# Performance work log

Measured on AMD Instinct MI355X. Metric: run time of the kernel, lower is better.

Reference implementation:

```python
import jax, jax.numpy as jnp
import numpy as np

NEG_SLOPE = 0.2
EPS = 1e-8

def add_self_loops(edge_index, n_nodes):
    loops = jnp.arange(n_nodes, dtype=edge_index.dtype)
    return jnp.concatenate([edge_index, jnp.stack([loops, loops])], axis=1)

def gatv2_layer(x, edge_index, Wl, Wr, att, bias, concat):
    # x: [N, Fin], edge_index: [2, E] (row0=src j, row1=dst i), att: [H, Fout]
    N = x.shape[0]
    H, Fo = att.shape
    ei = add_self_loops(edge_index, N)
    src, dst = ei[0], ei[1]
    xl = (x @ Wl).reshape(N, H, Fo)
    xr = (x @ Wr).reshape(N, H, Fo)
    s = xl[src] + xr[dst]                                   # [E, H, Fo]
    e = jnp.einsum('ehf,hf->eh', jax.nn.leaky_relu(s, NEG_SLOPE), att)  # [E, H]
    # segment softmax over edges sharing the same destination node
    m = jax.ops.segment_max(e, dst, num_segments=N)          # [N, H]
    ex = jnp.exp(e - m[dst])
    den = jax.ops.segment_sum(ex, dst, num_segments=N)
    alpha = ex / (den[dst] + 1e-16)                          # [E, H]
    out = jax.ops.segment_sum(xl[src] * alpha[:, :, None], dst, num_segments=N)  # [N, H, Fo]
    out = out.reshape(N, H * Fo) if concat else out.mean(axis=1)
    return out + bias

def forward_once(x, edge_index, W1l, W1r, att1, b1, W2l, W2r, att2, b2):
    # eval mode: dropouts are identity
    h = jax.nn.elu(gatv2_layer(x, edge_index, W1l, W1r, att1, b1, concat=True))
    return gatv2_layer(h, edge_index, W2l, W2r, att2, b2, concat=False)

def reference(x1, edge_index1, x2, edge_index2, W1l, W1r, att1, b1, W2l, W2r, att2, b2):
    y = forward_once(x1, edge_index1, W1l, W1r, att1, b1, W2l, W2r, att2, b2)
    z = forward_once(x2, edge_index2, W1l, W1r, att1, b1, W2l, W2r, att2, b2)
    logp_y = jax.nn.log_softmax(y, axis=1)
    logp_z = jax.nn.log_softmax(z, axis=1)
    ny = jnp.maximum(jnp.linalg.norm(y, axis=1), EPS)
    nz = jnp.maximum(jnp.linalg.norm(z, axis=1), EPS)
    cos = jnp.sum(y * z, axis=1) / (ny * nz)
    return (logp_y, 1.0 - cos, logp_z, logp_y, logp_y)

def setup_inputs() -> dict:
    key = jax.random.key(0)
    ks = jax.random.split(key, 12)
    N, E, Fin, HID, H, C = 50000, 800000, 256, 32, 8, 16
    g = lambda k, shape, fan: jax.random.normal(k, shape, jnp.float32) * (1.0 / np.sqrt(fan))
    return {
        'x1': jax.random.normal(ks[0], (N, Fin), jnp.float32),
        'edge_index1': jax.random.randint(ks[1], (2, E), 0, N, jnp.int32),
        'x2': jax.random.normal(ks[2], (N, Fin), jnp.float32),
        'edge_index2': jax.random.randint(ks[3], (2, E), 0, N, jnp.int32),
        'W1l': g(ks[4], (Fin, H * HID), Fin),
        'W1r': g(ks[5], (Fin, H * HID), Fin),
        'att1': g(ks[6], (H, HID), HID),
        'b1': jnp.zeros((H * HID,), jnp.float32),
        'W2l': g(ks[7], (H * HID, 1 * C), H * HID),
        'W2r': g(ks[8], (H * HID, 1 * C), H * HID),
        'att2': g(ks[9], (1, C), C),
        'b2': jnp.zeros((C,), jnp.float32),
    }
```

## Files before the change

### kernel.cpp

```cpp
#include <hip/hip_runtime.h>
#include <hip/hip_bf16.h>
#include <math.h>

#define FIN 256
#define C2  16
#define NEG 0.2f
#define LOG2E 1.4426950408889634f

typedef short bf16x8 __attribute__((ext_vector_type(8)));
typedef float f32x4v __attribute__((ext_vector_type(4)));
typedef float f32x2 __attribute__((ext_vector_type(2)));

__device__ __forceinline__ float bf2f(unsigned short u) {
  union { float f; unsigned int i; } c; c.i = ((unsigned int)u) << 16; return c.f;
}
__device__ __forceinline__ unsigned short f2bf(float f) {
  __hip_bfloat16 b = __float2bfloat16(f);
  return *(unsigned short*)&b;
}
__device__ __forceinline__ f32x2 bfpair(unsigned int u) {
  union { float f; unsigned int i; } lo, hi;
  lo.i = u << 16;
  hi.i = u & 0xffff0000u;
  f32x2 r; r.x = lo.f; r.y = hi.f; return r;
}

__global__ __launch_bounds__(256) void deg_kernel(const int* __restrict__ ei1,
    const int* __restrict__ ei2, int* __restrict__ deg, int E, int N) {
  int EQ = (E + 3) >> 2;
  int q = blockIdx.x * 256 + threadIdx.x;
  if (q >= 2 * EQ) return;
  int g = q >= EQ;
  int lq = g ? q - EQ : q;
  const int* dstp = (g ? ei2 : ei1) + E;
  int base = g * N;
  int e0 = lq * 4;
  if (e0 + 3 < E) {
    int4 d4 = *(const int4*)&dstp[e0];
    atomicAdd(&deg[base + d4.x], 1);
    atomicAdd(&deg[base + d4.y], 1);
    atomicAdd(&deg[base + d4.z], 1);
    atomicAdd(&deg[base + d4.w], 1);
  } else {
    for (int k = 0; k < 4 && e0 + k < E; k++)
      atomicAdd(&deg[base + dstp[e0 + k]], 1);
  }
}

__global__ __launch_bounds__(1024) void scan_part_kernel(const int* __restrict__ deg,
    int* __restrict__ offs, int* __restrict__ partials, int n) {
  __shared__ int wsum[16], wpref[16];
  int tid = threadIdx.x, lane = tid & 63, wid = tid >> 6;
  int idx = blockIdx.x * 1024 + tid;
  int v = (idx < n) ? deg[idx] : 0;
  int s = v;
#pragma unroll
  for (int o = 1; o < 64; o <<= 1) {
    int t = __shfl_up(s, o, 64);
    if (lane >= o) s += t;
  }
  if (lane == 63) wsum[wid] = s;
  __syncthreads();
  if (tid < 16) {
    int t = wsum[tid];
    int ss = t;
#pragma unroll
    for (int o = 1; o < 16; o <<= 1) {
      int u = __shfl_up(ss, o, 16);
      if (tid >= o) ss += u;
    }
    wpref[tid] = ss - t;
    if (tid == 15) partials[blockIdx.x] = ss;
  }
  __syncthreads();
  if (idx < n) offs[idx] = wpref[wid] + s - v;
}

__global__ __launch_bounds__(1024) void scan_fix_kernel(int* __restrict__ offs,
    const int* __restrict__ partials, int nb, int n) {
  __shared__ int wsum[16], wpref[16];
  __shared__ int carry_s;
  int tid = threadIdx.x, lane = tid & 63, wid = tid >> 6;
  int v = (tid < nb) ? partials[tid] : 0;
  int s = v;
#pragma unroll
  for (int o = 1; o < 64; o <<= 1) {
    int t = __shfl_up(s, o, 64);
    if (lane >= o) s += t;
  }
  if (lane == 63) wsum[wid] = s;
  __syncthreads();
  if (tid < 16) {
    int t = wsum[tid];
    int ss = t;
#pragma unroll
    for (int o = 1; o < 16; o <<= 1) {
      int u = __shfl_up(ss, o, 16);
      if (tid >= o) ss += u;
    }
    wpref[tid] = ss - t;
  }
  __syncthreads();
  s += wpref[wid];
  int b = blockIdx.x;
  if (b == 0) {
    if (tid == nb - 1) offs[n] = s;
  } else if (tid == b - 1) {
    carry_s = s;
  }
  __syncthreads();
  if (b > 0) {
    int idx = b * 1024 + tid;
    if (idx < n) offs[idx] += carry_s;
  }
}

__global__ __launch_bounds__(256) void fill_kernel(const int* __restrict__ ei1,
    const int* __restrict__ ei2, const int* __restrict__ offs,
    int* __restrict__ cnt, int* __restrict__ csr, int E, int N) {
  int EQ = (E + 3) >> 2;
  int q = blockIdx.x * 256 + threadIdx.x;
  if (q >= 2 * EQ) return;
  int g = q >= EQ;
  int lq = g ? q - EQ : q;
  const int* ei = g ? ei2 : ei1;
  int base = g * N;
  int e0 = lq * 4;
  if (e0 + 3 < E) {
    int4 s4 = *(const int4*)&ei[e0];
    int4 d4 = *(const int4*)&ei[E + e0];
    int n0 = base + d4.x, n1 = base + d4.y, n2 = base + d4.z, n3 = base + d4.w;
    csr[offs[n0] + atomicAdd(&cnt[n0], 1)] = base + s4.x;
    csr[offs[n1] + atomicAdd(&cnt[n1], 1)] = base + s4.y;
    csr[offs[n2] + atomicAdd(&cnt[n2], 1)] = base + s4.z;
    csr[offs[n3] + atomicAdd(&cnt[n3], 1)] = base + s4.w;
  } else {
    for (int k = 0; k < 4 && e0 + k < E; k++) {
      int node = base + ei[E + e0 + k];
      csr[offs[node] + atomicAdd(&cnt[node], 1)] = base + ei[e0 + k];
    }
  }
}

__global__ __launch_bounds__(256) void cvt_w_kernel(const float* __restrict__ W1l,
    const float* __restrict__ W1r, const float* __restrict__ W2l,
    const float* __restrict__ W2r, unsigned short* __restrict__ Wt,
    unsigned short* __restrict__ Wt2) {
  int n = blockIdx.x;
  int k = threadIdx.x;
  if (n < 512) {
    float v = (n < 256) ? W1l[k * 256 + n] : W1r[k * 256 + (n - 256)];
    Wt[n * 256 + k] = f2bf(v);
  } else {
    int c = n - 512;
    float v = (c < 16) ? W2l[k * 16 + c] : W2r[k * 16 + (c - 16)];
    Wt2[c * 256 + k] = f2bf(v);
  }
}

#define LDT 72
__global__ __launch_bounds__(512) void gemm_mfma_kernel(
    const float* __restrict__ X1, const float* __restrict__ X2,
    const unsigned short* __restrict__ Bt,
    unsigned short* __restrict__ xlb, unsigned short* __restrict__ xrb,
    int M, int NN) {
  __shared__ __align__(16) unsigned short As[128 * LDT];
  __shared__ __align__(16) unsigned short Bs[128 * LDT];
  int tid = threadIdx.x;
  int G = gridDim.x;
  int q = G >> 3, r = G & 7;
  int b = blockIdx.x;
  int xcd = b & 7, pos = b >> 3;
  int swz = (xcd < r) ? xcd * (q + 1) + pos : r * (q + 1) + (xcd - r) * q + pos;
  int row0 = (swz >> 2) * 128;
  int col0 = (swz & 3) * 128;
  int wid = tid >> 6, lane = tid & 63;
  int wr = wid >> 2, wc = wid & 3;
  int r16 = lane & 15, kb = (lane >> 4) * 8;

  f32x4v acc[4][2];
#pragma unroll
  for (int m = 0; m < 4; m++)
#pragma unroll
    for (int n = 0; n < 2; n++)
#pragma unroll
      for (int qq = 0; qq < 4; qq++) acc[m][n][qq] = 0.f;

  for (int k0 = 0; k0 < 256; k0 += 64) {
#pragma unroll
    for (int it = 0; it < 2; it++) {
      int g = tid + it * 512;
      int rr = g >> 3;
      int ko = (g & 7) * 8;
      int gr = row0 + rr;
      float4 a0 = make_float4(0.f, 0.f, 0.f, 0.f);
      float4 a1 = make_float4(0.f, 0.f, 0.f, 0.f);
      if (gr < M) {
        const float* src = (gr < NN) ? &X1[(size_t)gr * 256]
                                     : &X2[(size_t)(gr - NN) * 256];
        a0 = *(const float4*)&src[k0 + ko];
        a1 = *(const float4*)&src[k0 + ko + 4];
      }
      ushort4 lo, hi;
      lo.x = f2bf(a0.x); lo.y = f2bf(a0.y); lo.z = f2bf(a0.z); lo.w = f2bf(a0.w);
      hi.x = f2bf(a1.x); hi.y = f2bf(a1.y); hi.z = f2bf(a1.z); hi.w = f2bf(a1.w);
      *(ushort4*)&As[rr * LDT + ko] = lo;
      *(ushort4*)&As[rr * LDT + ko + 4] = hi;
      int4 bv = *(const int4*)&Bt[(size_t)(col0 + rr) * 256 + k0 + ko];
      *(int4*)&Bs[rr * LDT + ko] = bv;
    }
    __syncthreads();
#pragma unroll
    for (int kk = 0; kk < 64; kk += 32) {
      bf16x8 af[4], bfr[2];
#pragma unroll
      for (int m = 0; m < 4; m++)
        af[m] = *(const bf16x8*)&As[(wr * 64 + m * 16 + r16) * LDT + kk + kb];
#pragma unroll
      for (int n = 0; n < 2; n++)
        bfr[n] = *(const bf16x8*)&Bs[(wc * 32 + n * 16 + r16) * LDT + kk + kb];
#pragma unroll
      for (int m = 0; m < 4; m++)
#pragma unroll
        for (int n = 0; n < 2; n++)
          acc[m][n] = __builtin_amdgcn_mfma_f32_16x16x32_bf16(af[m], bfr[n], acc[m][n], 0, 0, 0);
    }
    __syncthreads();
  }
  unsigned short* Cb = (col0 < 256) ? xlb : xrb;
  int cbase = (col0 & 255) + wc * 32;
  int rq = (lane >> 4) * 4;
#pragma unroll
  for (int m = 0; m < 4; m++) {
#pragma unroll
    for (int n = 0; n < 2; n++) {
#pragma unroll
      for (int qq = 0; qq < 4; qq++) {
        int gr = row0 + wr * 64 + m * 16 + rq + qq;
        if (gr < M) {
          Cb[(size_t)gr * 256 + cbase + n * 16 + r16] = f2bf(acc[m][n][qq]);
        }
      }
    }
  }
}

#define LDB2 264
__global__ __launch_bounds__(256) void gemm2_mfma_kernel(
    const unsigned short* __restrict__ A, const unsigned short* __restrict__ Bt,
    unsigned short* __restrict__ xl2b, unsigned short* __restrict__ xr2b, int M) {
  __shared__ __align__(16) unsigned short As[256 * LDT];
  __shared__ __align__(16) unsigned short Bs[32 * LDB2];
  int tid = threadIdx.x;
  int row0 = blockIdx.x * 256;
  int wid = tid >> 6, lane = tid & 63;
  int r16 = lane & 15, kb = (lane >> 4) * 8, rq = (lane >> 4) * 4;

#pragma unroll
  for (int it = 0; it < 4; it++) {
    int g = tid + it * 256;
    int rr = g >> 5;
    int ko = (g & 31) * 8;
    *(int4*)&Bs[rr * LDB2 + ko] = *(const int4*)&Bt[rr * 256 + ko];
  }

  f32x4v acc[4][2];
#pragma unroll
  for (int m = 0; m < 4; m++)
#pragma unroll
    for (int n = 0; n < 2; n++)
#pragma unroll
      for (int qq = 0; qq < 4; qq++) acc[m][n][qq] = 0.f;

  for (int k0 = 0; k0 < 256; k0 += 64) {
#pragma unroll
    for (int it = 0; it < 8; it++) {
      int g = tid + it * 256;
      int rr = g >> 3;
      int ko = (g & 7) * 8;
      int gr = row0 + rr;
      int4 av = make_int4(0, 0, 0, 0);
      if (gr < M) av = *(const int4*)&A[(size_t)gr * 256 + k0 + ko];
      *(int4*)&As[rr * LDT + ko] = av;
    }
    __syncthreads();
#pragma unroll
    for (int kk = 0; kk < 64; kk += 32) {
      bf16x8 af[4], bfr[2];
#pragma unroll
      for (int m = 0; m < 4; m++)
        af[m] = *(const bf16x8*)&As[(wid * 64 + m * 16 + r16) * LDT + kk + kb];
#pragma unroll
      for (int n = 0; n < 2; n++)
        bfr[n] = *(const bf16x8*)&Bs[(n * 16 + r16) * LDB2 + k0 + kk + kb];
#pragma unroll
      for (int m = 0; m < 4; m++)
#pragma unroll
        for (int n = 0; n < 2; n++)
          acc[m][n] = __builtin_amdgcn_mfma_f32_16x16x32_bf16(af[m], bfr[n], acc[m][n], 0, 0, 0);
    }
    __syncthreads();
  }
#pragma unroll
  for (int m = 0; m < 4; m++) {
#pragma unroll
    for (int qq = 0; qq < 4; qq++) {
      int gr = row0 + wid * 64 + m * 16 + rq + qq;
      if (gr < M) {
        xl2b[(size_t)gr * 16 + r16] = f2bf(acc[m][0][qq]);
        xr2b[(size_t)gr * 16 + r16] = f2bf(acc[m][1][qq]);
      }
    }
  }
}

__global__ __launch_bounds__(256) void gat1_kernel(const unsigned short* __restrict__ xlb,
    unsigned short* xrb, const float* __restrict__ att, const float* __restrict__ bias,
    const int* __restrict__ offs, const int* __restrict__ csr, int M) {
  int w = threadIdx.x >> 6, lane = threadIdx.x & 63;
  int i = blockIdx.x * 4 + w;
  if (i >= M) return;
  i = __builtin_amdgcn_readfirstlane(i);
  const uint2* rows = (const uint2*)xlb;
  uint2 ul = rows[(size_t)i * 64 + lane];
  uint2 ur = ((const uint2*)(xrb + (size_t)i * 256))[lane];
  f32x2 xl01 = bfpair(ul.x), xl23 = bfpair(ul.y);
  f32x2 xr01 = bfpair(ur.x), xr23 = bfpair(ur.y);
  float4 a4 = ((const float4*)att)[lane];
  f32x2 a01; a01.x = a4.x * LOG2E; a01.y = a4.y * LOG2E;
  f32x2 a23; a23.x = a4.z * LOG2E; a23.y = a4.w * LOG2E;

  f32x2 t01 = xl01 + xr01, t23 = xl23 + xr23;
  f32x2 l01 = __builtin_elementwise_max(t01, t01 * NEG);
  f32x2 l23 = __builtin_elementwise_max(t23, t23 * NEG);
  f32x2 ps = l01 * a01 + l23 * a23;
  float p = ps.x + ps.y;
  p += __shfl_xor(p, 1, 8);
  p += __shfl_xor(p, 2, 8);
  p += __shfl_xor(p, 4, 8);
  float m = p, ssum = 1.f;
  f32x2 O01 = xl01, O23 = xl23;

  int e = offs[i], end = offs[i + 1];
  int rem = end - e;

  int ja0 = __builtin_amdgcn_readfirstlane(rem > 0 ? csr[e + 0] : i);
  int ja1 = __builtin_amdgcn_readfirstlane(rem > 1 ? csr[e + 1] : i);
  uint2 ua0 = rows[(size_t)ja0 * 64 + lane];
  uint2 ua1 = rows[(size_t)ja1 * 64 + lane];
  int jb0 = __builtin_amdgcn_readfirstlane(rem > 2 ? csr[e + 2] : i);
  int jb1 = __builtin_amdgcn_readfirstlane(rem > 3 ? csr[e + 3] : i);
  uint2 ub0 = rows[(size_t)jb0 * 64 + lane];
  uint2 ub1 = rows[(size_t)jb1 * 64 + lane];
  int jc0 = __builtin_amdgcn_readfirstlane(rem > 4 ? csr[e + 4] : i);
  int jc1 = __builtin_amdgcn_readfirstlane(rem > 5 ? csr[e + 5] : i);
  uint2 uc0 = rows[(size_t)jc0 * 64 + lane];
  uint2 uc1 = rows[(size_t)jc1 * 64 + lane];

  while (rem >= 2) {
    int jn0 = __builtin_amdgcn_readfirstlane(rem > 6 ? csr[e + 6] : i);
    int jn1 = __builtin_amdgcn_readfirstlane(rem > 7 ? csr[e + 7] : i);
    uint2 un0 = rows[(size_t)jn0 * 64 + lane];
    uint2 un1 = rows[(size_t)jn1 * 64 + lane];
    f32x2 x001 = bfpair(ua0.x), x023 = bfpair(ua0.y);
    f32x2 x101 = bfpair(ua1.x), x123 = bfpair(ua1.y);
    f32x2 q01 = x001 + xr01, q23 = x023 + xr23;
    f32x2 r01 = x101 + xr01, r23 = x123 + xr23;
    f32x2 g01 = __builtin_elementwise_max(q01, q01 * NEG);
    f32x2 g23 = __builtin_elementwise_max(q23, q23 * NEG);
    f32x2 k01 = __builtin_elementwise_max(r01, r01 * NEG);
    f32x2 k23 = __builtin_elementwise_max(r23, r23 * NEG);
    f32x2 s0v = g01 * a01 + g23 * a23;
    f32x2 s1v = k01 * a01 + k23 * a23;
    float p0 = s0v.x + s0v.y;
    float p1 = s1v.x + s1v.y;
    p0 += __shfl_xor(p0, 1, 8);
    p1 += __shfl_xor(p1, 1, 8);
    p0 += __shfl_xor(p0, 2, 8);
    p1 += __shfl_xor(p1, 2, 8);
    p0 += __shfl_xor(p0, 4, 8);
    p1 += __shfl_xor(p1, 4, 8);
    float mx = fmaxf(p0, p1);
    if (!__all(mx <= m + 8.f)) {
      float mn = fmaxf(m, mx);
      float sc = exp2f(m - mn);
      O01 *= sc; O23 *= sc; ssum *= sc; m = mn;
    }
    float w0 = exp2f(p0 - m), w1 = exp2f(p1 - m);
    O01 += w0 * x001 + w1 * x101;
    O23 += w0 * x023 + w1 * x123;
    ssum += w0 + w1;
    ua0 = ub0; ua1 = ub1;
    ub0 = uc0; ub1 = uc1;
    uc0 = un0; uc1 = un1;
    e += 2; rem -= 2;
  }
  if (rem == 1) {
    f32x2 x001 = bfpair(ua0.x), x023 = bfpair(ua0.y);
    f32x2 q01 = x001 + xr01, q23 = x023 + xr23;
    f32x2 g01 = __builtin_elementwise_max(q01, q01 * NEG);
    f32x2 g23 = __builtin_elementwise_max(q23, q23 * NEG);
    f32x2 s0v = g01 * a01 + g23 * a23;
    float p0 = s0v.x + s0v.y;
    p0 += __shfl_xor(p0, 1, 8);
    p0 += __shfl_xor(p0, 2, 8);
    p0 += __shfl_xor(p0, 4, 8);
    if (!__all(p0 <= m + 8.f)) {
      float mn = fmaxf(m, p0);
      float sc = exp2f(m - mn);
      O01 *= sc; O23 *= sc; ssum *= sc; m = mn;
    }
    float w0 = exp2f(p0 - m);
    O01 += w0 * x001;
    O23 += w0 * x023;
    ssum += w0;
  }
  float inv = 1.f / (ssum + 1e-16f);
  float4 b4 = ((const float4*)bias)[lane];
  float h0 = O01.x * inv + b4.x;
  float h1 = O01.y * inv + b4.y;
  float h2 = O23.x * inv + b4.z;
  float h3 = O23.y * inv + b4.w;
  h0 = h0 > 0.f ? h0 : (__expf(h0) - 1.f);
  h1 = h1 > 0.f ? h1 : (__expf(h1) - 1.f);
  h2 = h2 > 0.f ? h2 : (__expf(h2) - 1.f);
  h3 = h3 > 0.f ? h3 : (__expf(h3) - 1.f);
  ushort4 o;
  o.x = f2bf(h0); o.y = f2bf(h1); o.z = f2bf(h2); o.w = f2bf(h3);
  ((ushort4*)(xrb + (size_t)i * 256))[lane] = o;
}

__global__ __launch_bounds__(256) void gat2_kernel(const unsigned short* __restrict__ xl2b,
    const unsigned short* __restrict__ xr2b, const float* __restrict__ att,
    const float* __restrict__ b2, const int* __restrict__ offs,
    const int* __restrict__ csr, float* __restrict__ y2, int M) {
  int grp = threadIdx.x >> 4, c = threadIdx.x & 15;
  int i = blockIdx.x * 16 + grp;
  if (i >= M) return;
  float xli = bf2f(xl2b[(size_t)i * 16 + c]);
  float xri = bf2f(xr2b[(size_t)i * 16 + c]);
  float a = att[c] * LOG2E;
  float v = xli + xri; v = fmaxf(v, NEG * v);
  float p = v * a;
#pragma unroll
  for (int o = 8; o >= 1; o >>= 1) p += __shfl_xor(p, o, 16);
  float m = p, ssum = 1.0f, O = xli;

  int e = offs[i], end = offs[i + 1];
  int rem = end - e;

  int ja0 = rem > 0 ? csr[e + 0] : i;
  int ja1 = rem > 1 ? csr[e + 1] : i;
  float xa0 = bf2f(xl2b[(size_t)ja0 * 16 + c]);
  float xa1 = bf2f(xl2b[(size_t)ja1 * 16 + c]);
  int jb0 = rem > 2 ? csr[e + 2] : i;
  int jb1 = rem > 3 ? csr[e + 3] : i;
  float xb0 = bf2f(xl2b[(size_t)jb0 * 16 + c]);
  float xb1 = bf2f(xl2b[(size_t)jb1 * 16 + c]);
  int jc0 = rem > 4 ? csr[e + 4] : i;
  int jc1 = rem > 5 ? csr[e + 5] : i;
  float xc0 = bf2f(xl2b[(size_t)jc0 * 16 + c]);
  float xc1 = bf2f(xl2b[(size_t)jc1 * 16 + c]);

  while (rem >= 2) {
    int jn0 = rem > 6 ? csr[e + 6] : i;
    int jn1 = rem > 7 ? csr[e + 7] : i;
    float xn0 = bf2f(xl2b[(size_t)jn0 * 16 + c]);
    float xn1 = bf2f(xl2b[(size_t)jn1 * 16 + c]);
    float q0 = xa0 + xri; q0 = fmaxf(q0, NEG * q0);
    float q1 = xa1 + xri; q1 = fmaxf(q1, NEG * q1);
    float p0 = q0 * a, p1 = q1 * a;
#pragma unroll
    for (int o = 8; o >= 1; o >>= 1) {
      p0 += __shfl_xor(p0, o, 16);
      p1 += __shfl_xor(p1, o, 16);
    }
    float mx = fmaxf(p0, p1);
    if (!__all(mx <= m + 8.f)) {
      float mn = fmaxf(m, mx);
      float sc = exp2f(m - mn);
      O *= sc; ssum *= sc; m = mn;
    }
    float w0 = exp2f(p0 - m), w1 = exp2f(p1 - m);
    O += w0 * xa0 + w1 * xa1;
    ssum += w0 + w1;
    xa0 = xb0; xa1 = xb1;
    xb0 = xc0; xb1 = xc1;
    xc0 = xn0; xc1 = xn1;
    e += 2; rem -= 2;
  }
  if (rem == 1) {
    float q0 = xa0 + xri; q0 = fmaxf(q0, NEG * q0);
    float p0 = q0 * a;
#pragma unroll
    for (int o = 8; o >= 1; o >>= 1) p0 += __shfl_xor(p0, o, 16);
    if (!__all(p0 <= m + 8.f)) {
      float mn = fmaxf(m, p0);
      float sc = exp2f(m - mn);
      O *= sc; ssum *= sc; m = mn;
    }
    float w0 = exp2f(p0 - m);
    O += w0 * xa0;
    ssum += w0;
  }
  y2[(size_t)i * C2 + c] = O / (ssum + 1e-16f) + b2[c];
}

__global__ __launch_bounds__(256) void finalize_kernel(const float* __restrict__ y,
    const float* __restrict__ z, float* __restrict__ out, int N) {
  int grp = threadIdx.x >> 4, c = threadIdx.x & 15;
  int i = blockIdx.x * 16 + grp;
  if (i >= N) return;
  float yv = y[(size_t)i * C2 + c];
  float zv = z[(size_t)i * C2 + c];
  float my = yv;
#pragma unroll
  for (int o = 8; o >= 1; o >>= 1) my = fmaxf(my, __shfl_xor(my, o, 16));
  float sy = __expf(yv - my);
#pragma unroll
  for (int o = 8; o >= 1; o >>= 1) sy += __shfl_xor(sy, o, 16);
  float lpy = yv - my - __logf(sy);
  float mz = zv;
#pragma unroll
  for (int o = 8; o >= 1; o >>= 1) mz = fmaxf(mz, __shfl_xor(mz, o, 16));
  float sz = __expf(zv - mz);
#pragma unroll
  for (int o = 8; o >= 1; o >>= 1) sz += __shfl_xor(sz, o, 16);
  float lpz = zv - mz - __logf(sz);
  float dot = yv * zv, ny2 = yv * yv, nz2 = zv * zv;
#pragma unroll
  for (int o = 8; o >= 1; o >>= 1) {
    dot += __shfl_xor(dot, o, 16);
    ny2 += __shfl_xor(ny2, o, 16);
    nz2 += __shfl_xor(nz2, o, 16);
  }
  float ny = fmaxf(sqrtf(ny2), 1e-8f);
  float nz = fmaxf(sqrtf(nz2), 1e-8f);
  float cosv = dot / (ny * nz);
  size_t o1 = (size_t)N * C2;
  size_t o2 = o1 + N;
  size_t o3 = o2 + (size_t)N * C2;
  size_t o4 = o3 + (size_t)N * C2;
  size_t idx = (size_t)i * C2 + c;
  out[idx] = lpy;
  if (c == 0) out[o1 + i] = 1.0f - cosv;
  out[o2 + idx] = lpz;
  out[o3 + idx] = lpy;
  out[o4 + idx] = lpy;
}

extern "C" void kernel_launch(void* const* d_in, const int* in_sizes, int n_in,
                              void* d_out, int out_size, void* d_ws, size_t ws_size,
                              hipStream_t stream) {
  const float* x1   = (const float*)d_in[0];
  const int*   ei1  = (const int*)d_in[1];
  const float* x2   = (const float*)d_in[2];
  const int*   ei2  = (const int*)d_in[3];
  const float* W1l  = (const float*)d_in[4];
  const float* W1r  = (const float*)d_in[5];
  const float* att1 = (const float*)d_in[6];
  const float* b1   = (const float*)d_in[7];
  const float* W2l  = (const float*)d_in[8];
  const float* W2r  = (const float*)d_in[9];
  const float* att2 = (const float*)d_in[10];
  const float* b2   = (const float*)d_in[11];
  const int N = in_sizes[0] / FIN;
  const int E = in_sizes[1] / 2;
  const int M = 2 * N;
  float* out = (float*)d_out;

  char* w = (char*)d_ws;
  size_t off = 0;
  auto carve = [&](size_t bytes) -> void* {
    void* p = w + off;
    off += (bytes + 255) & ~(size_t)255;
    return p;
  };
  unsigned short* xlb  = (unsigned short*)carve((size_t)M * 256 * 2);
  unsigned short* xrb  = (unsigned short*)carve((size_t)M * 256 * 2);
  unsigned short* Wt   = (unsigned short*)carve(512 * 256 * 2);
  unsigned short* Wt2  = (unsigned short*)carve(32 * 256 * 2);
  unsigned short* xl2b = (unsigned short*)carve((size_t)M * 16 * 2);
  unsigned short* xr2b = (unsigned short*)carve((size_t)M * 16 * 2);
  float* y2  = (float*)carve((size_t)M * 16 * 4);
  int* deg  = (int*)carve((size_t)M * 4);
  int* cnt  = (int*)carve((size_t)M * 4);
  int* offs = (int*)carve((size_t)(M + 1) * 4);
  int* csr  = (int*)carve((size_t)2 * E * 4);
  int* partials = (int*)carve(128 * 4);
  (void)ws_size; (void)n_in; (void)out_size;

  const size_t zero_bytes = (size_t)((char*)cnt - (char*)deg) + (size_t)M * 4;
  hipMemsetAsync(deg, 0, zero_bytes, stream);

  const int NB = (M + 1023) / 1024;
  const int EQ = (E + 3) >> 2;

  cvt_w_kernel<<<544, 256, 0, stream>>>(W1l, W1r, W2l, W2r, Wt, Wt2);

  deg_kernel<<<(2 * EQ + 255) / 256, 256, 0, stream>>>(ei1, ei2, deg, E, N);
  scan_part_kernel<<<NB, 1024, 0, stream>>>(deg, offs, partials, M);
  scan_fix_kernel<<<NB, 1024, 0, stream>>>(offs, partials, NB, M);
  fill_kernel<<<(2 * EQ + 255) / 256, 256, 0, stream>>>(ei1, ei2, offs, cnt, csr, E, N);

  int RB = (M + 127) / 128;
  gemm_mfma_kernel<<<RB * 4, 512, 0, stream>>>(x1, x2, Wt, xlb, xrb, M, N);
  gat1_kernel<<<(M + 3) / 4, 256, 0, stream>>>(xlb, xrb, att1, b1, offs, csr, M);
  gemm2_mfma_kernel<<<(M + 255) / 256, 256, 0, stream>>>(xrb, Wt2, xl2b, xr2b, M);
  gat2_kernel<<<(M + 15) / 16, 256, 0, stream>>>(xl2b, xr2b, att2, b2, offs, csr, y2, M);

  finalize_kernel<<<(N + 15) / 16, 256, 0, stream>>>(y2, y2 + (size_t)N * 16, out, N);
}
```

Before: 410.9 us.

## Overlap CSR degree and fill passes with halves of layer-1 GEMM

```diff
diff --git a/kernel.cpp b/kernel.cpp
--- a/kernel.cpp
+++ b/kernel.cpp
@@ -25,154 +25,18 @@
   f32x2 r; r.x = lo.f; r.y = hi.f; return r;
 }
 
-__global__ __launch_bounds__(256) void deg_kernel(const int* __restrict__ ei1,
-    const int* __restrict__ ei2, int* __restrict__ deg, int E, int N) {
-  int EQ = (E + 3) >> 2;
-  int q = blockIdx.x * 256 + threadIdx.x;
-  if (q >= 2 * EQ) return;
-  int g = q >= EQ;
-  int lq = g ? q - EQ : q;
-  const int* dstp = (g ? ei2 : ei1) + E;
-  int base = g * N;
-  int e0 = lq * 4;
-  if (e0 + 3 < E) {
-    int4 d4 = *(const int4*)&dstp[e0];
-    atomicAdd(&deg[base + d4.x], 1);
-    atomicAdd(&deg[base + d4.y], 1);
-    atomicAdd(&deg[base + d4.z], 1);
-    atomicAdd(&deg[base + d4.w], 1);
-  } else {
-    for (int k = 0; k < 4 && e0 + k < E; k++)
-      atomicAdd(&deg[base + dstp[e0 + k]], 1);
-  }
-}
-
-__global__ __launch_bounds__(1024) void scan_part_kernel(const int* __restrict__ deg,
-    int* __restrict__ offs, int* __restrict__ partials, int n) {
-  __shared__ int wsum[16], wpref[16];
-  int tid = threadIdx.x, lane = tid & 63, wid = tid >> 6;
-  int idx = blockIdx.x * 1024 + tid;
-  int v = (idx < n) ? deg[idx] : 0;
-  int s = v;
-#pragma unroll
-  for (int o = 1; o < 64; o <<= 1) {
-    int t = __shfl_up(s, o, 64);
-    if (lane >= o) s += t;
-  }
-  if (lane == 63) wsum[wid] = s;
-  __syncthreads();
-  if (tid < 16) {
-    int t = wsum[tid];
-    int ss = t;
-#pragma unroll
-    for (int o = 1; o < 16; o <<= 1) {
-      int u = __shfl_up(ss, o, 16);
-      if (tid >= o) ss += u;
-    }
-    wpref[tid] = ss - t;
-    if (tid == 15) partials[blockIdx.x] = ss;
-  }
-  __syncthreads();
-  if (idx < n) offs[idx] = wpref[wid] + s - v;
-}
-
-__global__ __launch_bounds__(1024) void scan_fix_kernel(int* __restrict__ offs,
-    const int* __restrict__ partials, int nb, int n) {
-  __shared__ int wsum[16], wpref[16];
-  __shared__ int carry_s;
-  int tid = threadIdx.x, lane = tid & 63, wid = tid >> 6;
-  int v = (tid < nb) ? partials[tid] : 0;
-  int s = v;
-#pragma unroll
-  for (int o = 1; o < 64; o <<= 1) {
-    int t = __shfl_up(s, o, 64);
-    if (lane >= o) s += t;
-  }
-  if (lane == 63) wsum[wid] = s;
-  __syncthreads();
-  if (tid < 16) {
-    int t = wsum[tid];
-    int ss = t;
-#pragma unroll
-    for (int o = 1; o < 16; o <<= 1) {
-      int u = __shfl_up(ss, o, 16);
-      if (tid >= o) ss += u;
-    }
-    wpref[tid] = ss - t;
-  }
-  __syncthreads();
-  s += wpref[wid];
-  int b = blockIdx.x;
-  if (b == 0) {
-    if (tid == nb - 1) offs[n] = s;
-  } else if (tid == b - 1) {
-    carry_s = s;
-  }
-  __syncthreads();
-  if (b > 0) {
-    int idx = b * 1024 + tid;
-    if (idx < n) offs[idx] += carry_s;
-  }
-}
-
-__global__ __launch_bounds__(256) void fill_kernel(const int* __restrict__ ei1,
-    const int* __restrict__ ei2, const int* __restrict__ offs,
-    int* __restrict__ cnt, int* __restrict__ csr, int E, int N) {
-  int EQ = (E + 3) >> 2;
-  int q = blockIdx.x * 256 + threadIdx.x;
-  if (q >= 2 * EQ) return;
-  int g = q >= EQ;
-  int lq = g ? q - EQ : q;
-  const int* ei = g ? ei2 : ei1;
-  int base = g * N;
-  int e0 = lq * 4;
-  if (e0 + 3 < E) {
-    int4 s4 = *(const int4*)&ei[e0];
-    int4 d4 = *(const int4*)&ei[E + e0];
-    int n0 = base + d4.x, n1 = base + d4.y, n2 = base + d4.z, n3 = base + d4.w;
-    csr[offs[n0] + atomicAdd(&cnt[n0], 1)] = base + s4.x;
-    csr[offs[n1] + atomicAdd(&cnt[n1], 1)] = base + s4.y;
-    csr[offs[n2] + atomicAdd(&cnt[n2], 1)] = base + s4.z;
-    csr[offs[n3] + atomicAdd(&cnt[n3], 1)] = base + s4.w;
-  } else {
-    for (int k = 0; k < 4 && e0 + k < E; k++) {
-      int node = base + ei[E + e0 + k];
-      csr[offs[node] + atomicAdd(&cnt[node], 1)] = base + ei[e0 + k];
-    }
-  }
-}
-
-__global__ __launch_bounds__(256) void cvt_w_kernel(const float* __restrict__ W1l,
-    const float* __restrict__ W1r, const float* __restrict__ W2l,
-    const float* __restrict__ W2r, unsigned short* __restrict__ Wt,
-    unsigned short* __restrict__ Wt2) {
-  int n = blockIdx.x;
-  int k = threadIdx.x;
-  if (n < 512) {
-    float v = (n < 256) ? W1l[k * 256 + n] : W1r[k * 256 + (n - 256)];
-    Wt[n * 256 + k] = f2bf(v);
-  } else {
-    int c = n - 512;
-    float v = (c < 16) ? W2l[k * 16 + c] : W2r[k * 16 + (c - 16)];
-    Wt2[c * 256 + k] = f2bf(v);
-  }
-}
-
 #define LDT 72
-__global__ __launch_bounds__(512) void gemm_mfma_kernel(
-    const float* __restrict__ X1, const float* __restrict__ X2,
-    const unsigned short* __restrict__ Bt,
+__device__ __forceinline__ void gemm_tile(const float* __restrict__ X1,
+    const float* __restrict__ X2, const unsigned short* __restrict__ Bt,
     unsigned short* __restrict__ xlb, unsigned short* __restrict__ xrb,
-    int M, int NN) {
+    int M, int NN, int tileIdx, int G, int rowTileOff) {
   __shared__ __align__(16) unsigned short As[128 * LDT];
   __shared__ __align__(16) unsigned short Bs[128 * LDT];
   int tid = threadIdx.x;
-  int G = gridDim.x;
   int q = G >> 3, r = G & 7;
-  int b = blockIdx.x;
-  int xcd = b & 7, pos = b >> 3;
+  int xcd = tileIdx & 7, pos = tileIdx >> 3;
   int swz = (xcd < r) ? xcd * (q + 1) + pos : r * (q + 1) + (xcd - r) * q + pos;
-  int row0 = (swz >> 2) * 128;
+  int row0 = (rowTileOff + (swz >> 2)) * 128;
   int col0 = (swz & 3) * 128;
   int wid = tid >> 6, lane = tid & 63;
   int wr = wid >> 2, wc = wid & 3;
@@ -242,6 +106,155 @@
         }
       }
     }
+  }
+}
+
+__global__ __launch_bounds__(512) void deg_gemm_kernel(const int* __restrict__ ei1,
+    const int* __restrict__ ei2, int* __restrict__ deg, int E, int N, int degBlocks,
+    const float* __restrict__ X1, const float* __restrict__ X2,
+    const unsigned short* __restrict__ Bt,
+    unsigned short* __restrict__ xlb, unsigned short* __restrict__ xrb,
+    int M, int G, int rowTileOff) {
+  if ((int)blockIdx.x < degBlocks) {
+    int EQ = (E + 3) >> 2;
+    int q = blockIdx.x * 512 + threadIdx.x;
+    if (q >= 2 * EQ) return;
+    int g = q >= EQ;
+    int lq = g ? q - EQ : q;
+    const int* dstp = (g ? ei2 : ei1) + E;
+    int base = g * N;
+    int e0 = lq * 4;
+    if (e0 + 3 < E) {
+      int4 d4 = *(const int4*)&dstp[e0];
+      atomicAdd(&deg[base + d4.x], 1);
+      atomicAdd(&deg[base + d4.y], 1);
+      atomicAdd(&deg[base + d4.z], 1);
+      atomicAdd(&deg[base + d4.w], 1);
+    } else {
+      for (int k = 0; k < 4 && e0 + k < E; k++)
+        atomicAdd(&deg[base + dstp[e0 + k]], 1);
+    }
+  } else {
+    gemm_tile(X1, X2, Bt, xlb, xrb, M, N, blockIdx.x - degBlocks, G, rowTileOff);
+  }
+}
+
+__global__ __launch_bounds__(512) void fill_gemm_kernel(const int* __restrict__ ei1,
+    const int* __restrict__ ei2, const int* __restrict__ offs,
+    int* __restrict__ cnt, int* __restrict__ csr, int E, int N, int fillBlocks,
+    const float* __restrict__ X1, const float* __restrict__ X2,
+    const unsigned short* __restrict__ Bt,
+    unsigned short* __restrict__ xlb, unsigned short* __restrict__ xrb,
+    int M, int G, int rowTileOff) {
+  if ((int)blockIdx.x < fillBlocks) {
+    int EQ = (E + 3) >> 2;
+    int q = blockIdx.x * 512 + threadIdx.x;
+    if (q >= 2 * EQ) return;
+    int g = q >= EQ;
+    int lq = g ? q - EQ : q;
+    const int* ei = g ? ei2 : ei1;
+    int base = g * N;
+    int e0 = lq * 4;
+    if (e0 + 3 < E) {
+      int4 s4 = *(const int4*)&ei[e0];
+      int4 d4 = *(const int4*)&ei[E + e0];
+      int n0 = base + d4.x, n1 = base + d4.y, n2 = base + d4.z, n3 = base + d4.w;
+      csr[offs[n0] + atomicAdd(&cnt[n0], 1)] = base + s4.x;
+      csr[offs[n1] + atomicAdd(&cnt[n1], 1)] = base + s4.y;
+      csr[offs[n2] + atomicAdd(&cnt[n2], 1)] = base + s4.z;
+      csr[offs[n3] + atomicAdd(&cnt[n3], 1)] = base + s4.w;
+    } else {
+      for (int k = 0; k < 4 && e0 + k < E; k++) {
+        int node = base + ei[E + e0 + k];
+        csr[offs[node] + atomicAdd(&cnt[node], 1)] = base + ei[e0 + k];
+      }
+    }
+  } else {
+    gemm_tile(X1, X2, Bt, xlb, xrb, M, N, blockIdx.x - fillBlocks, G, rowTileOff);
+  }
+}
+
+__global__ __launch_bounds__(1024) void scan_part_kernel(const int* __restrict__ deg,
+    int* __restrict__ offs, int* __restrict__ partials, int n) {
+  __shared__ int wsum[16], wpref[16];
+  int tid = threadIdx.x, lane = tid & 63, wid = tid >> 6;
+  int idx = blockIdx.x * 1024 + tid;
+  int v = (idx < n) ? deg[idx] : 0;
+  int s = v;
+#pragma unroll
+  for (int o = 1; o < 64; o <<= 1) {
+    int t = __shfl_up(s, o, 64);
+    if (lane >= o) s += t;
+  }
+  if (lane == 63) wsum[wid] = s;
+  __syncthreads();
+  if (tid < 16) {
+    int t = wsum[tid];
+    int ss = t;
+#pragma unroll
+    for (int o = 1; o < 16; o <<= 1) {
+      int u = __shfl_up(ss, o, 16);
+      if (tid >= o) ss += u;
+    }
+    wpref[tid] = ss - t;
+    if (tid == 15) partials[blockIdx.x] = ss;
+  }
+  __syncthreads();
+  if (idx < n) offs[idx] = wpref[wid] + s - v;
+}
+
+__global__ __launch_bounds__(1024) void scan_fix_kernel(int* __restrict__ offs,
+    const int* __restrict__ partials, int nb, int n) {
+  __shared__ int wsum[16], wpref[16];
+  __shared__ int carry_s;
+  int tid = threadIdx.x, lane = tid & 63, wid = tid >> 6;
+  int v = (tid < nb) ? partials[tid] : 0;
+  int s = v;
+#pragma unroll
+  for (int o = 1; o < 64; o <<= 1) {
+    int t = __shfl_up(s, o, 64);
+    if (lane >= o) s += t;
+  }
+  if (lane == 63) wsum[wid] = s;
+  __syncthreads();
+  if (tid < 16) {
+    int t = wsum[tid];
+    int ss = t;
+#pragma unroll
+    for (int o = 1; o < 16; o <<= 1) {
+      int u = __shfl_up(ss, o, 16);
+      if (tid >= o) ss += u;
+    }
+    wpref[tid] = ss - t;
+  }
+  __syncthreads();
+  s += wpref[wid];
+  int b = blockIdx.x;
+  if (b == 0) {
+    if (tid == nb - 1) offs[n] = s;
+  } else if (tid == b - 1) {
+    carry_s = s;
+  }
+  __syncthreads();
+  if (b > 0) {
+    int idx = b * 1024 + tid;
+    if (idx < n) offs[idx] += carry_s;
+  }
+}
+
+__global__ __launch_bounds__(256) void cvt_w_kernel(const float* __restrict__ W1l,
+    const float* __restrict__ W1r, const float* __restrict__ W2l,
+    const float* __restrict__ W2r, unsigned short* __restrict__ Wt,
+    unsigned short* __restrict__ Wt2) {
+  int n = blockIdx.x;
+  int k = threadIdx.x;
+  if (n < 512) {
+    float v = (n < 256) ? W1l[k * 256 + n] : W1r[k * 256 + (n - 256)];
+    Wt[n * 256 + k] = f2bf(v);
+  } else {
+    int c = n - 512;
+    float v = (c < 16) ? W2l[k * 16 + c] : W2r[k * 16 + (c - 16)];
+    Wt2[c * 256 + k] = f2bf(v);
   }
 }
 
@@ -595,16 +608,23 @@
 
   const int NB = (M + 1023) / 1024;
   const int EQ = (E + 3) >> 2;
+  const int edgeBlocks = (2 * EQ + 511) / 512;
+
+  const int RB = (M + 127) / 128;
+  const int half1 = (RB + 1) / 2;
+  const int half2 = RB - half1;
+  const int G1 = half1 * 4;
+  const int G2 = half2 * 4;
 
   cvt_w_kernel<<<544, 256, 0, stream>>>(W1l, W1r, W2l, W2r, Wt, Wt2);
 
-  deg_kernel<<<(2 * EQ + 255) / 256, 256, 0, stream>>>(ei1, ei2, deg, E, N);
+  deg_gemm_kernel<<<edgeBlocks + G1, 512, 0, stream>>>(
+      ei1, ei2, deg, E, N, edgeBlocks, x1, x2, Wt, xlb, xrb, M, G1, 0);
   scan_part_kernel<<<NB, 1024, 0, stream>>>(deg, offs, partials, M);
   scan_fix_kernel<<<NB, 1024, 0, stream>>>(offs, partials, NB, M);
-  fill_kernel<<<(2 * EQ + 255) / 256, 256, 0, stream>>>(ei1, ei2, offs, cnt, csr, E, N);
-
-  int RB = (M + 127) / 128;
-  gemm_mfma_kernel<<<RB * 4, 512, 0, stream>>>(x1, x2, Wt, xlb, xrb, M, N);
+  fill_gemm_kernel<<<edgeBlocks + G2, 512, 0, stream>>>(
+      ei1, ei2, offs, cnt, csr, E, N, edgeBlocks, x1, x2, Wt, xlb, xrb, M, G2, half1);
+
   gat1_kernel<<<(M + 3) / 4, 256, 0, stream>>>(xlb, xrb, att1, b1, offs, csr, M);
   gemm2_mfma_kernel<<<(M + 255) / 256, 256, 0, stream>>>(xrb, Wt2, xl2b, xr2b, M);
   gat2_kernel<<<(M + 15) / 16, 256, 0, stream>>>(xl2b, xr2b, att2, b2, offs, csr, y2, M);
```

Result: no change. 413.3 us (+0.6%).

## Load GEMM A tiles via global_load_lds and seed CSR cursors from offsets

Applied to the files above, without the earlier changes.

```diff
diff --git a/kernel.cpp b/kernel.cpp
--- a/kernel.cpp
+++ b/kernel.cpp
@@ -77,7 +77,7 @@
 }
 
 __global__ __launch_bounds__(1024) void scan_fix_kernel(int* __restrict__ offs,
-    const int* __restrict__ partials, int nb, int n) {
+    int* __restrict__ cnt, const int* __restrict__ partials, int nb, int n) {
   __shared__ int wsum[16], wpref[16];
   __shared__ int carry_s;
   int tid = threadIdx.x, lane = tid & 63, wid = tid >> 6;
@@ -104,20 +104,23 @@
   s += wpref[wid];
   int b = blockIdx.x;
   if (b == 0) {
+    if (tid == 0) carry_s = 0;
     if (tid == nb - 1) offs[n] = s;
   } else if (tid == b - 1) {
     carry_s = s;
   }
   __syncthreads();
-  if (b > 0) {
-    int idx = b * 1024 + tid;
-    if (idx < n) offs[idx] += carry_s;
+  int idx = b * 1024 + tid;
+  if (idx < n) {
+    int val = offs[idx] + carry_s;
+    offs[idx] = val;
+    cnt[idx] = val;
   }
 }
 
 __global__ __launch_bounds__(256) void fill_kernel(const int* __restrict__ ei1,
-    const int* __restrict__ ei2, const int* __restrict__ offs,
-    int* __restrict__ cnt, int* __restrict__ csr, int E, int N) {
+    const int* __restrict__ ei2, int* __restrict__ cnt, int* __restrict__ csr,
+    int E, int N) {
   int EQ = (E + 3) >> 2;
   int q = blockIdx.x * 256 + threadIdx.x;
   if (q >= 2 * EQ) return;
@@ -129,15 +132,14 @@
   if (e0 + 3 < E) {
     int4 s4 = *(const int4*)&ei[e0];
     int4 d4 = *(const int4*)&ei[E + e0];
-    int n0 = base + d4.x, n1 = base + d4.y, n2 = base + d4.z, n3 = base + d4.w;
-    csr[offs[n0] + atomicAdd(&cnt[n0], 1)] = base + s4.x;
-    csr[offs[n1] + atomicAdd(&cnt[n1], 1)] = base + s4.y;
-    csr[offs[n2] + atomicAdd(&cnt[n2], 1)] = base + s4.z;
-    csr[offs[n3] + atomicAdd(&cnt[n3], 1)] = base + s4.w;
+    csr[atomicAdd(&cnt[base + d4.x], 1)] = base + s4.x;
+    csr[atomicAdd(&cnt[base + d4.y], 1)] = base + s4.y;
+    csr[atomicAdd(&cnt[base + d4.z], 1)] = base + s4.z;
+    csr[atomicAdd(&cnt[base + d4.w], 1)] = base + s4.w;
   } else {
     for (int k = 0; k < 4 && e0 + k < E; k++) {
       int node = base + ei[E + e0 + k];
-      csr[offs[node] + atomicAdd(&cnt[node], 1)] = base + ei[e0 + k];
+      csr[atomicAdd(&cnt[node], 1)] = base + ei[e0 + k];
     }
   }
 }
@@ -159,12 +161,13 @@
 }
 
 #define LDT 72
+#define AGS 260
 __global__ __launch_bounds__(512) void gemm_mfma_kernel(
     const float* __restrict__ X1, const float* __restrict__ X2,
     const unsigned short* __restrict__ Bt,
     unsigned short* __restrict__ xlb, unsigned short* __restrict__ xrb,
     int M, int NN) {
-  __shared__ __align__(16) unsigned short As[128 * LDT];
+  __shared__ __align__(16) float As[32 * AGS];
   __shared__ __align__(16) unsigned short Bs[128 * LDT];
   int tid = threadIdx.x;
   int G = gridDim.x;
@@ -177,6 +180,8 @@
   int wid = tid >> 6, lane = tid & 63;
   int wr = wid >> 2, wc = wid & 3;
   int r16 = lane & 15, kb = (lane >> 4) * 8;
+  int lrow = lane >> 4;
+  int lchunk = lane & 15;
 
   f32x4v acc[4][2];
 #pragma unroll
@@ -192,30 +197,39 @@
       int g = tid + it * 512;
       int rr = g >> 3;
       int ko = (g & 7) * 8;
-      int gr = row0 + rr;
-      float4 a0 = make_float4(0.f, 0.f, 0.f, 0.f);
-      float4 a1 = make_float4(0.f, 0.f, 0.f, 0.f);
-      if (gr < M) {
-        const float* src = (gr < NN) ? &X1[(size_t)gr * 256]
-                                     : &X2[(size_t)(gr - NN) * 256];
-        a0 = *(const float4*)&src[k0 + ko];
-        a1 = *(const float4*)&src[k0 + ko + 4];
-      }
-      ushort4 lo, hi;
-      lo.x = f2bf(a0.x); lo.y = f2bf(a0.y); lo.z = f2bf(a0.z); lo.w = f2bf(a0.w);
-      hi.x = f2bf(a1.x); hi.y = f2bf(a1.y); hi.z = f2bf(a1.z); hi.w = f2bf(a1.w);
-      *(ushort4*)&As[rr * LDT + ko] = lo;
-      *(ushort4*)&As[rr * LDT + ko + 4] = hi;
       int4 bv = *(const int4*)&Bt[(size_t)(col0 + rr) * 256 + k0 + ko];
       *(int4*)&Bs[rr * LDT + ko] = bv;
     }
+#pragma unroll
+    for (int it = 0; it < 4; it++) {
+      int g = wid * 4 + it;
+      int gr = row0 + g * 4 + lrow;
+      if (gr > M - 1) gr = M - 1;
+      const float* src = (gr < NN) ? (X1 + (size_t)gr * 256)
+                                   : (X2 + (size_t)(gr - NN) * 256);
+      src += k0 + lchunk * 4;
+      __builtin_amdgcn_global_load_lds(
+          (const __attribute__((address_space(1))) unsigned int*)src,
+          (__attribute__((address_space(3))) unsigned int*)&As[g * AGS],
+          16, 0, 0);
+    }
     __syncthreads();
 #pragma unroll
     for (int kk = 0; kk < 64; kk += 32) {
       bf16x8 af[4], bfr[2];
 #pragma unroll
-      for (int m = 0; m < 4; m++)
-        af[m] = *(const bf16x8*)&As[(wr * 64 + m * 16 + r16) * LDT + kk + kb];
+      for (int m = 0; m < 4; m++) {
+        int rrow = wr * 64 + m * 16 + r16;
+        const float* ap = &As[rrow * 64 + (rrow >> 2) * 4 + kk + kb];
+        float4 f0 = *(const float4*)ap;
+        float4 f1 = *(const float4*)(ap + 4);
+        union { bf16x8 v; unsigned short u[8]; } pk;
+        pk.u[0] = f2bf(f0.x); pk.u[1] = f2bf(f0.y);
+        pk.u[2] = f2bf(f0.z); pk.u[3] = f2bf(f0.w);
+        pk.u[4] = f2bf(f1.x); pk.u[5] = f2bf(f1.y);
+        pk.u[6] = f2bf(f1.z); pk.u[7] = f2bf(f1.w);
+        af[m] = pk.v;
+      }
 #pragma unroll
       for (int n = 0; n < 2; n++)
         bfr[n] = *(const bf16x8*)&Bs[(wc * 32 + n * 16 + r16) * LDT + kk + kb];
@@ -590,8 +604,7 @@
   int* partials = (int*)carve(128 * 4);
   (void)ws_size; (void)n_in; (void)out_size;
 
-  const size_t zero_bytes = (size_t)((char*)cnt - (char*)deg) + (size_t)M * 4;
-  hipMemsetAsync(deg, 0, zero_bytes, stream);
+  hipMemsetAsync(deg, 0, (size_t)M * 4, stream);
 
   const int NB = (M + 1023) / 1024;
   const int EQ = (E + 3) >> 2;
@@ -600,8 +613,8 @@
 
   deg_kernel<<<(2 * EQ + 255) / 256, 256, 0, stream>>>(ei1, ei2, deg, E, N);
   scan_part_kernel<<<NB, 1024, 0, stream>>>(deg, offs, partials, M);
-  scan_fix_kernel<<<NB, 1024, 0, stream>>>(offs, partials, NB, M);
-  fill_kernel<<<(2 * EQ + 255) / 256, 256, 0, stream>>>(ei1, ei2, offs, cnt, csr, E, N);
+  scan_fix_kernel<<<NB, 1024, 0, stream>>>(offs, cnt, partials, NB, M);
+  fill_kernel<<<(2 * EQ + 255) / 256, 256, 0, stream>>>(ei1, ei2, cnt, csr, E, N);
 
   int RB = (M + 127) / 128;
   gemm_mfma_kernel<<<RB * 4, 512, 0, stream>>>(x1, x2, Wt, xlb, xrb, M, N);
```

Result: slower. 556.6 us (+35.5%).
